# Optimization experiments

Hardware: AMD Instinct MI355X
Metric: run time of the kernel (lower is better)

Reference implementation:

```python
import jax, jax.numpy as jnp
import numpy as np

N_QUBITS = 8
DEPTH = 3


def _apply_1q(state, U, q):
    # state: (2,)*n complex, apply 2x2 unitary U on qubit axis q
    state = jnp.moveaxis(state, q, -1)
    state = state @ U.T
    return jnp.moveaxis(state, -1, q)


def _ry(state, theta, q):
    h = theta * 0.5
    c, s = jnp.cos(h), jnp.sin(h)
    U = jnp.stack([jnp.stack([c, -s]), jnp.stack([s, c])]).astype(jnp.complex64)
    return _apply_1q(state, U, q)


def _rz(state, theta, q):
    h = theta * 0.5
    d = jnp.stack([jnp.exp(-1j * h), jnp.exp(1j * h)]).astype(jnp.complex64)
    state = jnp.moveaxis(state, q, -1) * d
    return jnp.moveaxis(state, -1, q)


def _cx(state, c, t):
    # CNOT with control c, target t: flip target amplitudes where control=1
    state = jnp.moveaxis(state, (c, t), (-2, -1))
    s0 = state[..., 0, :]
    s1 = state[..., 1, ::-1]
    state = jnp.stack([s0, s1], axis=-2)
    return jnp.moveaxis(state, (-2, -1), (c, t))


def _simulate(angles, qparams):
    # Single-sample circuit: RY angle encoding, then DEPTH layers of (RZ,RY) per
    # qubit + CX ring. Returns <Z_0> (Hamiltonian 'Z' + 'I'*(n-1)).
    state = jnp.zeros((2,) * N_QUBITS, jnp.complex64).at[(0,) * N_QUBITS].set(1.0)
    for q in range(N_QUBITS):
        state = _ry(state, angles[q], q)
    idx = 0
    for _ in range(DEPTH):
        for q in range(N_QUBITS):
            state = _rz(state, qparams[idx], q); idx += 1
            state = _ry(state, qparams[idx], q); idx += 1
        for i in range(N_QUBITS):
            state = _cx(state, i, (i + 1) % N_QUBITS)
    probs = jnp.abs(state) ** 2
    return probs[0].sum() - probs[1].sum()


def setup_inputs() -> dict:
    key = jax.random.key(0)
    ks = jax.random.split(key, 6)
    B, F, H = 16384, 16, 256
    nq = 2 * N_QUBITS * DEPTH  # 48 variational params
    return {
        "x": jax.random.normal(ks[0], (B, F), jnp.float32),
        "enc_w1": jax.random.normal(ks[1], (H, F), jnp.float32) / np.sqrt(F).astype(np.float32),
        "enc_b1": jnp.zeros((H,), jnp.float32),
        "enc_w2": jax.random.normal(ks[2], (N_QUBITS, H), jnp.float32) / np.sqrt(H).astype(np.float32),
        "enc_b2": jnp.zeros((N_QUBITS,), jnp.float32),
        "qparams": jax.random.normal(ks[3], (nq,), jnp.float32) * 0.1,
        "dec_w1": jax.random.normal(ks[4], (H, 1), jnp.float32),
        "dec_b1": jnp.zeros((H,), jnp.float32),
        "dec_w2": jax.random.normal(ks[5], (1, H), jnp.float32) / np.sqrt(H).astype(np.float32),
        "dec_b2": jnp.zeros((1,), jnp.float32),
    }


def reference(x, enc_w1, enc_b1, enc_w2, enc_b2, qparams, dec_w1, dec_b1, dec_w2, dec_b2):
    # encoder: Linear -> ReLU -> Linear -> Tanh, scaled by pi (angle encoding)
    h = jax.nn.relu(x @ enc_w1.T + enc_b1)
    angles = jnp.tanh(h @ enc_w2.T + enc_b2) * jnp.pi  # (B, n_qubits)
    # vectorized quantum state-vector simulation over the batch
    expvals = jax.vmap(_simulate, in_axes=(0, None))(angles, qparams)  # (B,)
    q = expvals[:, None]  # (B, 1)
    # decoder: Linear(1->H) -> ReLU -> Linear(H->1) -> Sigmoid
    d = jax.nn.relu(q @ dec_w1.T + dec_b1)
    return jax.nn.sigmoid(d @ dec_w2.T + dec_b2)
```

## Files before the change

### kernel.cpp

```cpp
#include <hip/hip_runtime.h>
#include <math.h>

#define NQ 8
#define DEPTH 3
#define FDIM 16
#define HDIM 256
#define WAVES_PER_BLOCK 4
#define THREADS (WAVES_PER_BLOCK * 64)
#define ROWS_PER_BLOCK (WAVES_PER_BLOCK * 2)
#define NGATE (NQ * DEPTH)

template<int CTRL>
__device__ __forceinline__ float dpp1(float v) {
    return __int_as_float(__builtin_amdgcn_update_dpp(
        0, __float_as_int(v), CTRL, 0xF, 0xF, true));
}

template<int M4>
__device__ __forceinline__ float shuf4(float v) {
    if constexpr (M4 == 1)  return dpp1<0xB1>(v);
    else if constexpr (M4 == 2)  return dpp1<0x4E>(v);
    else if constexpr (M4 == 4)  return dpp1<0x1B>(dpp1<0x141>(v));
    else if constexpr (M4 == 8)  return dpp1<0x128>(v);
    else return v;
}

template<int ML>
__device__ __forceinline__ float shuf(float v, int lane) {
    if constexpr (ML == 0) {
        return v;
    } else if constexpr (ML >= 32) {
        int addr = (lane ^ ML) << 2;
        return __int_as_float(__builtin_amdgcn_ds_bpermute(addr, __float_as_int(v)));
    } else {
        return __int_as_float(__builtin_amdgcn_ds_swizzle(
            __float_as_int(v), (ML << 10) | 0x1F));
    }
}

__device__ __forceinline__ float wred(float v, int lane) {
    v += shuf4<1>(v);
    v += shuf4<2>(v);
    v += shuf4<4>(v);
    v += shuf4<8>(v);
#if __has_builtin(__builtin_amdgcn_permlane16_swap)
    {
        auto r = __builtin_amdgcn_permlane16_swap(__float_as_int(v), __float_as_int(v), false, false);
        v = __int_as_float(r[0]) + __int_as_float(r[1]);
    }
#else
    v += __shfl_xor(v, 16, 64);
#endif
#if __has_builtin(__builtin_amdgcn_permlane32_swap)
    {
        auto r = __builtin_amdgcn_permlane32_swap(__float_as_int(v), __float_as_int(v), false, false);
        v = __int_as_float(r[0]) + __int_as_float(r[1]);
    }
#else
    v += __shfl_xor(v, 32, 64);
#endif
    return v;
}

__device__ __forceinline__ float fast_tanh(float y) {
    float ex = __expf(2.f * y);
    return 1.f - 2.f * __builtin_amdgcn_rcpf(ex + 1.f);
}

template<int M, int R>
__device__ __forceinline__ void gate_m(float (&srA)[4], float (&siA)[4],
                                       float (&srB)[4], float (&siB)[4],
                                       float a0, float a1, float b0, float b1,
                                       int lane) {
    constexpr int ML = M & 63, MH = (M >> 6) & 3;
    constexpr int RL = R & 63, RH = (R >> 6) & 3;
    bool p0;
    if constexpr (RL == 0)                 p0 = false;
    else if constexpr ((RL & (RL-1)) == 0) p0 = (lane & RL) != 0;
    else                                   p0 = (__popc(lane & RL) & 1) != 0;

    float prA[4], piA[4], prB[4], piB[4];
#pragma unroll
    for (int hi = 0; hi < 4; hi++) {
        prA[hi] = shuf<ML>(srA[hi ^ MH], lane);
        piA[hi] = shuf<ML>(siA[hi ^ MH], lane);
        prB[hi] = shuf<ML>(srB[hi ^ MH], lane);
        piB[hi] = shuf<ML>(siB[hi ^ MH], lane);
    }

    float ea1 = p0 ? a1 : -a1;
    float eb0 = p0 ? b0 : -b0;

#pragma unroll
    for (int hi = 0; hi < 4; hi++) {
        const bool f = (__builtin_popcount(hi & RH) & 1) != 0;
        float za1 = f ? -ea1 : ea1;
        float zb0 = f ? -eb0 : eb0;
        float lrA = fmaf(-za1, siA[hi], a0 * srA[hi]);
        float liA = fmaf( za1, srA[hi], a0 * siA[hi]);
        srA[hi] = fmaf( b1, piA[hi], fmaf(zb0, prA[hi], lrA));
        siA[hi] = fmaf(-b1, prA[hi], fmaf(zb0, piA[hi], liA));
        float lrB = fmaf(-za1, siB[hi], a0 * srB[hi]);
        float liB = fmaf( za1, srB[hi], a0 * siB[hi]);
        srB[hi] = fmaf( b1, piB[hi], fmaf(zb0, prB[hi], lrB));
        siB[hi] = fmaf(-b1, prB[hi], fmaf(zb0, piB[hi], liB));
    }
}

__global__ __launch_bounds__(THREADS, 4) void hqcl_kernel(
    const float* __restrict__ x,
    const float* __restrict__ w1,
    const float* __restrict__ b1,
    const float* __restrict__ w2,
    const float* __restrict__ b2,
    const float* __restrict__ qp,
    const float* __restrict__ dw1,
    const float* __restrict__ db1,
    const float* __restrict__ dw2,
    const float* __restrict__ db2,
    float* __restrict__ out, int B)
{
    __shared__ float4 sG4[NGATE];

    const int t = threadIdx.x;
    if (t < NGATE) {
        float cz, sz, cy, sy;
        __sincosf(qp[2 * t] * 0.5f,     &sz, &cz);
        __sincosf(qp[2 * t + 1] * 0.5f, &sy, &cy);
        sG4[t] = make_float4(cz * cy, sz * cy, cz * sy, sz * sy);
    }
    __syncthreads();

    const int lane = t & 63;
    const int row0 = blockIdx.x * ROWS_PER_BLOCK + (t >> 6) * 2;
    if (row0 >= B) return;
    const int rowB = (row0 + 1 < B) ? row0 + 1 : row0;

    const float4* xA = (const float4*)(x + row0 * FDIM);
    const float4* xB = (const float4*)(x + rowB * FDIM);
    float4 xa0 = xA[0], xa1 = xA[1], xa2 = xA[2], xa3 = xA[3];
    float4 xb0 = xB[0], xb1 = xB[1], xb2 = xB[2], xb3 = xB[3];

    float hA[4], hB[4];
#pragma unroll
    for (int m = 0; m < 4; m++) {
        int j = lane + 64 * m;
        const float4* wp = (const float4*)(w1 + j * FDIM);
        float4 wa = wp[0], wb = wp[1], wc = wp[2], wd = wp[3];
        float bv = b1[j];
        float aA = bv, aB = bv;
        aA = fmaf(xa0.x, wa.x, aA); aA = fmaf(xa0.y, wa.y, aA);
        aA = fmaf(xa0.z, wa.z, aA); aA = fmaf(xa0.w, wa.w, aA);
        aA = fmaf(xa1.x, wb.x, aA); aA = fmaf(xa1.y, wb.y, aA);
        aA = fmaf(xa1.z, wb.z, aA); aA = fmaf(xa1.w, wb.w, aA);
        aA = fmaf(xa2.x, wc.x, aA); aA = fmaf(xa2.y, wc.y, aA);
        aA = fmaf(xa2.z, wc.z, aA); aA = fmaf(xa2.w, wc.w, aA);
        aA = fmaf(xa3.x, wd.x, aA); aA = fmaf(xa3.y, wd.y, aA);
        aA = fmaf(xa3.z, wd.z, aA); aA = fmaf(xa3.w, wd.w, aA);
        aB = fmaf(xb0.x, wa.x, aB); aB = fmaf(xb0.y, wa.y, aB);
        aB = fmaf(xb0.z, wa.z, aB); aB = fmaf(xb0.w, wa.w, aB);
        aB = fmaf(xb1.x, wb.x, aB); aB = fmaf(xb1.y, wb.y, aB);
        aB = fmaf(xb1.z, wb.z, aB); aB = fmaf(xb1.w, wb.w, aB);
        aB = fmaf(xb2.x, wc.x, aB); aB = fmaf(xb2.y, wc.y, aB);
        aB = fmaf(xb2.z, wc.z, aB); aB = fmaf(xb2.w, wc.w, aB);
        aB = fmaf(xb3.x, wd.x, aB); aB = fmaf(xb3.y, wd.y, aB);
        aB = fmaf(xb3.z, wd.z, aB); aB = fmaf(xb3.w, wd.w, aB);
        hA[m] = fmaxf(aA, 0.f);
        hB[m] = fmaxf(aB, 0.f);
    }

    float c0A, s0A, c1A, s1A, c0B, s0B, c1B, s1B;
    float plA = 1.f, plB = 1.f;
#pragma unroll
    for (int q = 0; q < NQ; q++) {
        float aA = 0.f, aB = 0.f;
#pragma unroll
        for (int m = 0; m < 4; m++) {
            float wv = w2[q * HDIM + lane + 64 * m];
            aA = fmaf(hA[m], wv, aA);
            aB = fmaf(hB[m], wv, aB);
        }
        aA = wred(aA, lane);
        aB = wred(aB, lane);
        float bq = b2[q];
        float uA = 0.25f * fast_tanh(aA + bq);
        float uB = 0.25f * fast_tanh(aB + bq);
        float svA, cvA, svB, cvB;
        asm("v_sin_f32 %0, %1" : "=v"(svA) : "v"(uA));
        asm("v_cos_f32 %0, %1" : "=v"(cvA) : "v"(uA));
        asm("v_sin_f32 %0, %1" : "=v"(svB) : "v"(uB));
        asm("v_cos_f32 %0, %1" : "=v"(cvB) : "v"(uB));
        if (q == 0)      { c0A = cvA; s0A = svA; c0B = cvB; s0B = svB; }
        else if (q == 1) { c1A = cvA; s1A = svA; c1B = cvB; s1B = svB; }
        else {
            bool bit = (lane >> (7 - q)) & 1;
            plA *= bit ? svA : cvA;
            plB *= bit ? svB : cvB;
        }
    }

    float srA[4], siA[4], srB[4], siB[4];
    srA[0] = plA * c1A * c0A;  srA[1] = plA * s1A * c0A;
    srA[2] = plA * c1A * s0A;  srA[3] = plA * s1A * s0A;
    srB[0] = plB * c1B * c0B;  srB[1] = plB * s1B * c0B;
    srB[2] = plB * c1B * s0B;  srB[3] = plB * s1B * s0B;
#pragma unroll
    for (int hi = 0; hi < 4; hi++) { siA[hi] = 0.f; siB[hi] = 0.f; }

#define GATE(L, Q, MM, RR) { float4 g4 = sG4[(L)*8 + (Q)]; \
        gate_m<MM, RR>(srA, siA, srB, siB, g4.x, g4.y, g4.z, g4.w, lane); }
    GATE(0,0,0x80,0x80) GATE(0,1,0x40,0x40) GATE(0,2,0x20,0x20) GATE(0,3,0x10,0x10)
    GATE(0,4,0x08,0x08) GATE(0,5,0x04,0x04) GATE(0,6,0x02,0x02) GATE(0,7,0x01,0x01)
    GATE(1,0,0xC0,0x7F) GATE(1,1,0x60,0xC0) GATE(1,2,0x30,0xE0) GATE(1,3,0x18,0xF0)
    GATE(1,4,0x0C,0xF8) GATE(1,5,0x06,0xFC) GATE(1,6,0x03,0xFE) GATE(1,7,0xC1,0xFF)
    GATE(2,0,0xA0,0xD5) GATE(2,1,0x50,0xBF) GATE(2,2,0x28,0x5F) GATE(2,3,0x14,0xAF)
    GATE(2,4,0x0A,0x57) GATE(2,5,0x05,0xAB) GATE(2,6,0xC2,0x55) GATE(2,7,0x61,0xAA)
#undef GATE

    bool pb = (__popc(lane & 0x0C) & 1) != 0;
    float m0A = srA[0]*srA[0] + siA[0]*siA[0] + srA[2]*srA[2] + siA[2]*siA[2];
    float m1A = srA[1]*srA[1] + siA[1]*siA[1] + srA[3]*srA[3] + siA[3]*siA[3];
    float m0B = srB[0]*srB[0] + siB[0]*siB[0] + srB[2]*srB[2] + siB[2]*siB[2];
    float m1B = srB[1]*srB[1] + siB[1]*siB[1] + srB[3]*srB[3] + siB[3]*siB[3];
    float eA = pb ? (m1A - m0A) : (m0A - m1A);
    float eB = pb ? (m1B - m0B) : (m0B - m1B);
    eA = wred(eA, lane);
    eB = wred(eB, lane);

    float accA = 0.f, accB = 0.f;
#pragma unroll
    for (int m = 0; m < 4; m++) {
        int j = lane + 64 * m;
        float w1v = dw1[j], bv = db1[j], w2v = dw2[j];
        float dA = fmaxf(fmaf(eA, w1v, bv), 0.f);
        float dB = fmaxf(fmaf(eB, w1v, bv), 0.f);
        accA = fmaf(dA, w2v, accA);
        accB = fmaf(dB, w2v, accB);
    }
    accA = wred(accA, lane);
    accB = wred(accB, lane);
    if (lane == 0) {
        float bb = db2[0];
        out[row0] = 1.f / (1.f + __expf(-(accA + bb)));
        if (row0 + 1 < B)
            out[row0 + 1] = 1.f / (1.f + __expf(-(accB + bb)));
    }
}

extern "C" void kernel_launch(void* const* d_in, const int* in_sizes, int n_in,
                              void* d_out, int out_size, void* d_ws, size_t ws_size,
                              hipStream_t stream) {
    const float* x   = (const float*)d_in[0];
    const float* w1  = (const float*)d_in[1];
    const float* b1  = (const float*)d_in[2];
    const float* w2  = (const float*)d_in[3];
    const float* b2  = (const float*)d_in[4];
    const float* qp  = (const float*)d_in[5];
    const float* dw1 = (const float*)d_in[6];
    const float* db1 = (const float*)d_in[7];
    const float* dw2 = (const float*)d_in[8];
    const float* db2 = (const float*)d_in[9];
    float* out = (float*)d_out;

    const int B = in_sizes[0] / FDIM;
    const int grid = (B + ROWS_PER_BLOCK - 1) / ROWS_PER_BLOCK;
    hqcl_kernel<<<grid, THREADS, 0, stream>>>(x, w1, b1, w2, b2, qp, dw1, db1, dw2, db2, out, B);
}
```

Measured before the change: 39.22 us.

## Pack two samples per wave as 32-lane halves with 8 amplitudes per lane

The state layout changes from each wave holding two full 256-amplitude states (4 per lane per sample) to each 32-lane half-wave holding one sample, with 8 amplitudes per lane. Cross-lane gate partners now use DPP row ops and permlane16 swaps instead of ds_swizzle/ds_bpermute, which removes LDS-path shuffles. The final expectation reduction splits between the halves using permlane32. This adds more in-register index permutation and composed two-step DPP ops, and changes how bits are mapped to lanes.

After: 49.47 us. 26.1% more time.

```diff
diff --git a/kernel.cpp b/kernel.cpp
--- a/kernel.cpp
+++ b/kernel.cpp
@@ -17,32 +17,55 @@
 }
 
 template<int M4>
-__device__ __forceinline__ float shuf4(float v) {
-    if constexpr (M4 == 1)  return dpp1<0xB1>(v);
+__device__ __forceinline__ float dppx(float v) {
+    if constexpr (M4 == 0)  return v;
+    else if constexpr (M4 == 1)  return dpp1<0xB1>(v);
     else if constexpr (M4 == 2)  return dpp1<0x4E>(v);
+    else if constexpr (M4 == 3)  return dpp1<0x1B>(v);
     else if constexpr (M4 == 4)  return dpp1<0x1B>(dpp1<0x141>(v));
+    else if constexpr (M4 == 5)  return dpp1<0x4E>(dpp1<0x141>(v));
+    else if constexpr (M4 == 6)  return dpp1<0xB1>(dpp1<0x141>(v));
+    else if constexpr (M4 == 7)  return dpp1<0x141>(v);
     else if constexpr (M4 == 8)  return dpp1<0x128>(v);
-    else return v;
+    else if constexpr (M4 == 9)  return dpp1<0xB1>(dpp1<0x128>(v));
+    else if constexpr (M4 == 10) return dpp1<0x4E>(dpp1<0x128>(v));
+    else if constexpr (M4 == 11) return dpp1<0x1B>(dpp1<0x128>(v));
+    else if constexpr (M4 == 12) return dpp1<0x1B>(dpp1<0x140>(v));
+    else if constexpr (M4 == 13) return dpp1<0x4E>(dpp1<0x140>(v));
+    else if constexpr (M4 == 14) return dpp1<0xB1>(dpp1<0x140>(v));
+    else                         return dpp1<0x140>(v);
+}
+
+__device__ __forceinline__ float px16v(float v, int lane) {
+#if __has_builtin(__builtin_amdgcn_permlane16_swap)
+    auto r = __builtin_amdgcn_permlane16_swap(__float_as_int(v), __float_as_int(v), false, false);
+    return __int_as_float((lane & 16) ? r[0] : r[1]);
+#else
+    return __shfl_xor(v, 16, 64);
+#endif
+}
+__device__ __forceinline__ float px32v(float v, int lane) {
+#if __has_builtin(__builtin_amdgcn_permlane32_swap)
+    auto r = __builtin_amdgcn_permlane32_swap(__float_as_int(v), __float_as_int(v), false, false);
+    return __int_as_float((lane & 32) ? r[0] : r[1]);
+#else
+    return __shfl_xor(v, 32, 64);
+#endif
 }
 
 template<int ML>
-__device__ __forceinline__ float shuf(float v, int lane) {
-    if constexpr (ML == 0) {
-        return v;
-    } else if constexpr (ML >= 32) {
-        int addr = (lane ^ ML) << 2;
-        return __int_as_float(__builtin_amdgcn_ds_bpermute(addr, __float_as_int(v)));
-    } else {
-        return __int_as_float(__builtin_amdgcn_ds_swizzle(
-            __float_as_int(v), (ML << 10) | 0x1F));
-    }
+__device__ __forceinline__ float shuf5(float v, int lane) {
+    float r = v;
+    if constexpr ((ML & 15) != 0) r = dppx<ML & 15>(r);
+    if constexpr ((ML & 16) != 0) r = px16v(r, lane);
+    return r;
 }
 
 __device__ __forceinline__ float wred(float v, int lane) {
-    v += shuf4<1>(v);
-    v += shuf4<2>(v);
-    v += shuf4<4>(v);
-    v += shuf4<8>(v);
+    v += dppx<1>(v);
+    v += dppx<2>(v);
+    v += dppx<4>(v);
+    v += dppx<8>(v);
 #if __has_builtin(__builtin_amdgcn_permlane16_swap)
     {
         auto r = __builtin_amdgcn_permlane16_swap(__float_as_int(v), __float_as_int(v), false, false);
@@ -68,42 +91,33 @@
 }
 
 template<int M, int R>
-__device__ __forceinline__ void gate_m(float (&srA)[4], float (&siA)[4],
-                                       float (&srB)[4], float (&siB)[4],
+__device__ __forceinline__ void gate32(float (&kr)[8], float (&ki)[8],
                                        float a0, float a1, float b0, float b1,
                                        int lane) {
-    constexpr int ML = M & 63, MH = (M >> 6) & 3;
-    constexpr int RL = R & 63, RH = (R >> 6) & 3;
+    constexpr int MK = (M >> 5) & 7, ML = M & 31;
+    constexpr int RK = (R >> 5) & 7, RL = R & 31;
     bool p0;
     if constexpr (RL == 0)                 p0 = false;
     else if constexpr ((RL & (RL-1)) == 0) p0 = (lane & RL) != 0;
     else                                   p0 = (__popc(lane & RL) & 1) != 0;
-
-    float prA[4], piA[4], prB[4], piB[4];
-#pragma unroll
-    for (int hi = 0; hi < 4; hi++) {
-        prA[hi] = shuf<ML>(srA[hi ^ MH], lane);
-        piA[hi] = shuf<ML>(siA[hi ^ MH], lane);
-        prB[hi] = shuf<ML>(srB[hi ^ MH], lane);
-        piB[hi] = shuf<ML>(siB[hi ^ MH], lane);
-    }
-
     float ea1 = p0 ? a1 : -a1;
     float eb0 = p0 ? b0 : -b0;
 
-#pragma unroll
-    for (int hi = 0; hi < 4; hi++) {
-        const bool f = (__builtin_popcount(hi & RH) & 1) != 0;
+    float pr[8], pi[8];
+#pragma unroll
+    for (int k = 0; k < 8; k++) {
+        pr[k] = shuf5<ML>(kr[k ^ MK], lane);
+        pi[k] = shuf5<ML>(ki[k ^ MK], lane);
+    }
+#pragma unroll
+    for (int k = 0; k < 8; k++) {
+        const bool f = (__builtin_popcount(k & RK) & 1) != 0;
         float za1 = f ? -ea1 : ea1;
         float zb0 = f ? -eb0 : eb0;
-        float lrA = fmaf(-za1, siA[hi], a0 * srA[hi]);
-        float liA = fmaf( za1, srA[hi], a0 * siA[hi]);
-        srA[hi] = fmaf( b1, piA[hi], fmaf(zb0, prA[hi], lrA));
-        siA[hi] = fmaf(-b1, prA[hi], fmaf(zb0, piA[hi], liA));
-        float lrB = fmaf(-za1, siB[hi], a0 * srB[hi]);
-        float liB = fmaf( za1, srB[hi], a0 * siB[hi]);
-        srB[hi] = fmaf( b1, piB[hi], fmaf(zb0, prB[hi], lrB));
-        siB[hi] = fmaf(-b1, prB[hi], fmaf(zb0, piB[hi], liB));
+        float lr = fmaf(-za1, ki[k], a0 * kr[k]);
+        float li = fmaf( za1, kr[k], a0 * ki[k]);
+        kr[k] = fmaf( b1, pi[k], fmaf(zb0, pr[k], lr));
+        ki[k] = fmaf(-b1, pr[k], fmaf(zb0, pi[k], li));
     }
 }
 
@@ -169,8 +183,8 @@
         hB[m] = fmaxf(aB, 0.f);
     }
 
-    float c0A, s0A, c1A, s1A, c0B, s0B, c1B, s1B;
-    float plA = 1.f, plB = 1.f;
+    float c0r, s0r, c1r, s1r, c2r, s2r;
+    float plg = 1.f;
 #pragma unroll
     for (int q = 0; q < NQ; q++) {
         float aA = 0.f, aB = 0.f;
@@ -190,25 +204,28 @@
         asm("v_cos_f32 %0, %1" : "=v"(cvA) : "v"(uA));
         asm("v_sin_f32 %0, %1" : "=v"(svB) : "v"(uB));
         asm("v_cos_f32 %0, %1" : "=v"(cvB) : "v"(uB));
-        if (q == 0)      { c0A = cvA; s0A = svA; c0B = cvB; s0B = svB; }
-        else if (q == 1) { c1A = cvA; s1A = svA; c1B = cvB; s1B = svB; }
-        else {
-            bool bit = (lane >> (7 - q)) & 1;
-            plA *= bit ? svA : cvA;
-            plB *= bit ? svB : cvB;
-        }
-    }
-
-    float srA[4], siA[4], srB[4], siB[4];
-    srA[0] = plA * c1A * c0A;  srA[1] = plA * s1A * c0A;
-    srA[2] = plA * c1A * s0A;  srA[3] = plA * s1A * s0A;
-    srB[0] = plB * c1B * c0B;  srB[1] = plB * s1B * c0B;
-    srB[2] = plB * c1B * s0B;  srB[3] = plB * s1B * s0B;
-#pragma unroll
-    for (int hi = 0; hi < 4; hi++) { siA[hi] = 0.f; siB[hi] = 0.f; }
+        float cq = (lane & 32) ? cvB : cvA;
+        float sq = (lane & 32) ? svB : svA;
+        if (q == 0)      { c0r = cq; s0r = sq; }
+        else if (q == 1) { c1r = cq; s1r = sq; }
+        else if (q == 2) { c2r = cq; s2r = sq; }
+        else             { plg *= ((lane >> (7 - q)) & 1) ? sq : cq; }
+    }
+
+    float pq[4];
+    pq[0] = plg * c0r * c1r;
+    pq[1] = plg * c0r * s1r;
+    pq[2] = plg * s0r * c1r;
+    pq[3] = plg * s0r * s1r;
+    float kr[8], ki[8];
+#pragma unroll
+    for (int k = 0; k < 8; k++) {
+        kr[k] = pq[k >> 1] * ((k & 1) ? s2r : c2r);
+        ki[k] = 0.f;
+    }
 
 #define GATE(L, Q, MM, RR) { float4 g4 = sG4[(L)*8 + (Q)]; \
-        gate_m<MM, RR>(srA, siA, srB, siB, g4.x, g4.y, g4.z, g4.w, lane); }
+        gate32<MM, RR>(kr, ki, g4.x, g4.y, g4.z, g4.w, lane); }
     GATE(0,0,0x80,0x80) GATE(0,1,0x40,0x40) GATE(0,2,0x20,0x20) GATE(0,3,0x10,0x10)
     GATE(0,4,0x08,0x08) GATE(0,5,0x04,0x04) GATE(0,6,0x02,0x02) GATE(0,7,0x01,0x01)
     GATE(1,0,0xC0,0x7F) GATE(1,1,0x60,0xC0) GATE(1,2,0x30,0xE0) GATE(1,3,0x18,0xF0)
@@ -217,15 +234,30 @@
     GATE(2,4,0x0A,0x57) GATE(2,5,0x05,0xAB) GATE(2,6,0xC2,0x55) GATE(2,7,0x61,0xAA)
 #undef GATE
 
-    bool pb = (__popc(lane & 0x0C) & 1) != 0;
-    float m0A = srA[0]*srA[0] + siA[0]*siA[0] + srA[2]*srA[2] + siA[2]*siA[2];
-    float m1A = srA[1]*srA[1] + siA[1]*siA[1] + srA[3]*srA[3] + siA[3]*siA[3];
-    float m0B = srB[0]*srB[0] + siB[0]*siB[0] + srB[2]*srB[2] + siB[2]*siB[2];
-    float m1B = srB[1]*srB[1] + siB[1]*siB[1] + srB[3]*srB[3] + siB[3]*siB[3];
-    float eA = pb ? (m1A - m0A) : (m0A - m1A);
-    float eB = pb ? (m1B - m0B) : (m0B - m1B);
-    eA = wred(eA, lane);
-    eB = wred(eB, lane);
+    float tp = 0.f, tn = 0.f;
+#pragma unroll
+    for (int k = 0; k < 8; k++) {
+        float m = fmaf(kr[k], kr[k], ki[k] * ki[k]);
+        if ((k >> 1) & 1) tn += m; else tp += m;
+    }
+    float tt = tp - tn;
+    bool pg = (__popc(lane & 0x0C) & 1) != 0;
+    float e = pg ? -tt : tt;
+    e += dppx<1>(e);
+    e += dppx<2>(e);
+    e += dppx<4>(e);
+    e += dppx<8>(e);
+#if __has_builtin(__builtin_amdgcn_permlane16_swap)
+    {
+        auto r = __builtin_amdgcn_permlane16_swap(__float_as_int(e), __float_as_int(e), false, false);
+        e = __int_as_float(r[0]) + __int_as_float(r[1]);
+    }
+#else
+    e += __shfl_xor(e, 16, 64);
+#endif
+    float eo = px32v(e, lane);
+    float eA = (lane & 32) ? eo : e;
+    float eB = (lane & 32) ? e : eo;
 
     float accA = 0.f, accB = 0.f;
 #pragma unroll
```
